# Optimization experiments

Measured on AMD Instinct MI355X. Metric: run time of the kernel, lower is better.

Reference implementation:

```python
import jax, jax.numpy as jnp
import numpy as np

B, S, D = 2, 2048, 2048
H, KVH, DH = 32, 8, 64
G = H // KVH  # num_key_value_groups
SCALE = DH ** -0.5
NEG = -1e9


def rotate_half(x):
    x1, x2 = jnp.split(x, 2, axis=-1)
    return jnp.concatenate([-x2, x1], axis=-1)


def setup_inputs() -> dict:
    key = jax.random.key(0)
    ks = jax.random.split(key, 6)
    hidden_states = jax.random.normal(ks[0], (B, S, D), dtype=jnp.float32)
    # RoPE tables (base 10000), shape [B, S, DH]
    inv_freq = 1.0 / (10000.0 ** (np.arange(0, DH, 2, dtype=np.float32) / DH))
    t = np.arange(S, dtype=np.float32)
    freqs = np.outer(t, inv_freq)                     # [S, DH/2]
    emb = np.concatenate([freqs, freqs], axis=-1)     # [S, DH]
    cos = jnp.broadcast_to(jnp.cos(emb)[None], (B, S, DH)).astype(jnp.float32)
    sin = jnp.broadcast_to(jnp.sin(emb)[None], (B, S, DH)).astype(jnp.float32)
    # additive causal mask [B, 1, S, S]
    causal = np.tril(np.ones((S, S), dtype=bool))
    mask = jnp.asarray(np.where(causal, 0.0, NEG).astype(np.float32))
    attention_mask = jnp.broadcast_to(mask[None, None], (B, 1, S, S))
    std = 0.02
    Wq = jax.random.normal(ks[1], (H * DH, D), dtype=jnp.float32) * std
    Wk = jax.random.normal(ks[2], (KVH * DH, D), dtype=jnp.float32) * std
    Wv = jax.random.normal(ks[3], (KVH * DH, D), dtype=jnp.float32) * std
    Wo = jax.random.normal(ks[4], (D, H * DH), dtype=jnp.float32) * std
    return {"hidden_states": hidden_states, "cos": cos, "sin": sin,
            "attention_mask": attention_mask, "Wq": Wq, "Wk": Wk, "Wv": Wv, "Wo": Wo}


def reference(hidden_states, cos, sin, attention_mask, Wq, Wk, Wv, Wo):
    b, s, d = hidden_states.shape
    # projections -> [B, heads, S, DH]
    q = (hidden_states @ Wq.T).reshape(b, s, H, DH).transpose(0, 2, 1, 3)
    k = (hidden_states @ Wk.T).reshape(b, s, KVH, DH).transpose(0, 2, 1, 3)
    v = (hidden_states @ Wv.T).reshape(b, s, KVH, DH).transpose(0, 2, 1, 3)
    # RoPE (unsqueeze_dim=1)
    c = cos[:, None]  # [B,1,S,DH]
    sn = sin[:, None]
    q = q * c + rotate_half(q) * sn
    k = k * c + rotate_half(k) * sn
    # GQA: repeat kv heads
    k = jnp.repeat(k, G, axis=1)
    v = jnp.repeat(v, G, axis=1)
    scores = jnp.einsum("bhqd,bhkd->bhqk", q, k) * SCALE + attention_mask
    attn = jax.nn.softmax(scores.astype(jnp.float32), axis=-1).astype(q.dtype)
    out = jnp.einsum("bhqk,bhkd->bhqd", attn, v)          # [B,H,S,DH]
    out = out.transpose(0, 2, 1, 3).reshape(b, s, H * DH)  # [B,S,H*DH]
    return out @ Wo.T
```

## Files before the change

kernel.cpp:

```cpp
#include <hip/hip_runtime.h>

typedef unsigned short u16;
typedef __attribute__((ext_vector_type(8))) short s16x8;
typedef __attribute__((ext_vector_type(4))) float f32x4;
typedef __attribute__((ext_vector_type(4))) unsigned short u16x4;

#define MFMA16(a, b, c) __builtin_amdgcn_mfma_f32_16x16x32_bf16(a, b, c, 0, 0, 0)

__device__ __forceinline__ u16 f2bf(float f) {
  unsigned u = __builtin_bit_cast(unsigned, f);
  u += 0x7fffu + ((u >> 16) & 1u);
  return (u16)(u >> 16);
}

__device__ __forceinline__ u16 f2bf_fast(float f) {
  return (u16)((__builtin_bit_cast(unsigned, f) + 0x8000u) >> 16);
}

__device__ __forceinline__ void async16(const void* g, void* l) {
  __builtin_amdgcn_global_load_lds(
      (const __attribute__((address_space(1))) void*)g,
      (__attribute__((address_space(3))) void*)l, 16, 0, 0);
}

__device__ __forceinline__ s16x8 ld8(const u16* p) { return *(const s16x8*)p; }

#define PRE 0.18033688011112042f

__global__ __launch_bounds__(256) void cvt_all(
    const float* __restrict__ X, const float* __restrict__ Wq,
    const float* __restrict__ Wk, const float* __restrict__ Wv,
    const float* __restrict__ Wo, u16* __restrict__ out) {
  long e = (long)(blockIdx.x * 256 + threadIdx.x) * 4;
  const float* src;
  if (e < 8388608L) src = X + e;
  else if (e < 12582912L) src = Wq + (e - 8388608L);
  else if (e < 13631488L) src = Wk + (e - 12582912L);
  else if (e < 14680064L) src = Wv + (e - 13631488L);
  else src = Wo + (e - 14680064L);
  float4 v = *(const float4*)src;
  u16x4 o = {f2bf(v.x), f2bf(v.y), f2bf(v.z), f2bf(v.w)};
  *(u16x4*)(out + e) = o;
}

enum { EPI_QKV = 0, EPI_OUT = 1 };

template <int EPI>
__global__ __launch_bounds__(256) void gemm_nt(
    const u16* __restrict__ A, const u16* __restrict__ Bm,
    const float* __restrict__ cosp, const float* __restrict__ sinp,
    u16* __restrict__ Qo, u16* __restrict__ Ko, u16* __restrict__ Vo,
    float* __restrict__ Co, int K) {
  __shared__ u16 SM[16384];
  const int t = threadIdx.x;
  const int lane = t & 63;
  const int w = t >> 6, wm = w >> 1, wn = w & 1;
  const int quad = lane >> 4, c16 = lane & 15;
  const int m0 = blockIdx.y * 128, n0 = blockIdx.x * 128;

  f32x4 acc[4][4];
  const f32x4 zero = {0.f, 0.f, 0.f, 0.f};
#pragma unroll
  for (int i = 0; i < 4; ++i)
#pragma unroll
    for (int j = 0; j < 4; ++j) acc[i][j] = zero;

  const u16* gA[2];
  const u16* gB[2];
  int lof[2];
#pragma unroll
  for (int p = 0; p < 2; ++p) {
    int c = t + p * 256;
    int dr = c >> 3, k8 = (c & 7) ^ (dr & 7);
    int row = 2 * dr + (k8 >> 2), col = (k8 & 3) * 8;
    gA[p] = A + (size_t)(m0 + row) * K + col;
    gB[p] = Bm + (size_t)(n0 + row) * K + col;
    lof[p] = c * 8;
  }

  int aoff[4], boff[4];
#pragma unroll
  for (int i = 0; i < 4; ++i) {
    int rowA = wm * 64 + i * 16 + c16;
    int drA = rowA >> 1;
    int chA = (((rowA & 1) << 2) | quad) ^ (drA & 7);
    aoff[i] = drA * 64 + chA * 8;
    int rowB = wn * 64 + i * 16 + c16;
    int drB = rowB >> 1;
    int chB = (((rowB & 1) << 2) | quad) ^ (drB & 7);
    boff[i] = 4096 + drB * 64 + chB * 8;
  }

#pragma unroll
  for (int p = 0; p < 2; ++p) {
    async16(gA[p], &SM[lof[p]]);
    async16(gB[p], &SM[4096 + lof[p]]);
  }

  const int niter = K >> 5;
  for (int kt = 0; kt < niter; ++kt) {
    const int cb = (kt & 1) * 8192;
    __syncthreads();
    if (kt + 1 < niter) {
      const int nb = 8192 - cb;
#pragma unroll
      for (int p = 0; p < 2; ++p) {
        gA[p] += 32;
        gB[p] += 32;
        async16(gA[p], &SM[nb + lof[p]]);
        async16(gB[p], &SM[nb + 4096 + lof[p]]);
      }
    }
    s16x8 af[4], bfr[4];
#pragma unroll
    for (int i = 0; i < 4; ++i) af[i] = ld8(&SM[cb + aoff[i]]);
#pragma unroll
    for (int j = 0; j < 4; ++j) bfr[j] = ld8(&SM[cb + boff[j]]);
#pragma unroll
    for (int i = 0; i < 4; ++i)
#pragma unroll
      for (int j = 0; j < 4; ++j) acc[i][j] = MFMA16(af[i], bfr[j], acc[i][j]);
  }

  if (EPI == EPI_OUT) {
#pragma unroll
    for (int i = 0; i < 4; ++i)
#pragma unroll
      for (int r = 0; r < 4; ++r) {
        int m = m0 + wm * 64 + i * 16 + quad * 4 + r;
        float* dst = Co + (size_t)m * 2048 + n0 + wn * 64 + c16;
#pragma unroll
        for (int j = 0; j < 4; ++j) dst[j * 16] = acc[i][j][r];
      }
  } else if (n0 >= 2560) {
    __syncthreads();
#pragma unroll
    for (int i = 0; i < 4; ++i)
#pragma unroll
      for (int r = 0; r < 4; ++r) {
        int sl = wm * 64 + i * 16 + quad * 4 + r;
#pragma unroll
        for (int j = 0; j < 4; ++j) {
          int dl = wn * 64 + j * 16 + c16;
          SM[dl * 128 + (((sl >> 3) ^ (dl & 15)) * 8) + (sl & 7)] =
              f2bf(acc[i][j][r]);
        }
      }
    __syncthreads();
    int bb = m0 >> 11, m0s = m0 & 2047;
#pragma unroll
    for (int p = 0; p < 8; ++p) {
      int q = p * 256 + t;
      int dl = q >> 4, k = q & 15;
      s16x8 vrow = ld8(&SM[dl * 128 + ((k ^ (dl & 15)) * 8)]);
      int nab = n0 + dl;
      int kvh = (nab - 2560) >> 6, dh = nab & 63;
      *(s16x8*)(Vo + ((size_t)(bb * 8 + kvh) * 64 + dh) * 2048 + m0s + k * 8) =
          vrow;
    }
  } else {
    const int nbase = n0 + wn * 64;
#pragma unroll
    for (int i = 0; i < 4; ++i)
#pragma unroll
      for (int r = 0; r < 4; ++r) {
        int m = m0 + wm * 64 + i * 16 + quad * 4 + r;
        int b = m >> 11, s = m & 2047;
        if (nbase < 2048) {
          int h = nbase >> 6;
          size_t base = ((size_t)(b * 32 + h) * 2048 + s) * 64;
#pragma unroll
          for (int j = 0; j < 2; ++j) {
            int d = j * 16 + c16;
            float v1 = acc[i][j][r], v2 = acc[i][j + 2][r];
            float c1 = cosp[m * 64 + d], s1 = sinp[m * 64 + d];
            float c2 = cosp[m * 64 + d + 32], s2 = sinp[m * 64 + d + 32];
            Qo[base + d] = f2bf((v1 * c1 - v2 * s1) * PRE);
            Qo[base + d + 32] = f2bf((v2 * c2 + v1 * s2) * PRE);
          }
        } else {
          int h = (nbase - 2048) >> 6;
          size_t base = ((size_t)(b * 8 + h) * 2048 + s) * 64;
#pragma unroll
          for (int j = 0; j < 2; ++j) {
            int d = j * 16 + c16;
            float v1 = acc[i][j][r], v2 = acc[i][j + 2][r];
            float c1 = cosp[m * 64 + d], s1 = sinp[m * 64 + d];
            float c2 = cosp[m * 64 + d + 32], s2 = sinp[m * 64 + d + 32];
            Ko[base + d] = f2bf(v1 * c1 - v2 * s1);
            Ko[base + d + 32] = f2bf(v2 * c2 + v1 * s2);
          }
        }
      }
  }
}

__global__ __launch_bounds__(256) void attn(const u16* __restrict__ Q,
                                            const u16* __restrict__ Kg,
                                            const u16* __restrict__ Vg,
                                            u16* __restrict__ O) {
  __shared__ u16 Ks[2][4096];
  __shared__ u16 Vs[2][4096];
  __shared__ u16 Ps[8192];
  const int t = threadIdx.x;
  const int lane = t & 63;
  const int w = t >> 6;
  const int quad = lane >> 4, c16 = lane & 15;
  const int bh = blockIdx.y;
  const int b = bh >> 5, h = bh & 31;
  const int kvh = h >> 2;

  const u16* Qbase = Q + ((size_t)(b * 32 + h) * 2048) * 64;
  const u16* Kbase = Kg + ((size_t)(b * 8 + kvh) * 2048) * 64;
  const u16* Vbase = Vg + ((size_t)(b * 8 + kvh) * 64) * 2048;

  const int sr0 = t >> 3, sc0 = ((t & 7) ^ (sr0 & 7)) * 8;
  const int sr1 = (t + 256) >> 3, sc1 = (((t + 256) & 7) ^ (sr1 & 7)) * 8;

  for (int ph = 0; ph < 2; ++ph) {
    const int qt = ph ? 15 - blockIdx.x : blockIdx.x;
    const int q0 = qt * 128;

    s16x8 qa[2][2];
#pragma unroll
    for (int im = 0; im < 2; ++im)
#pragma unroll
      for (int c = 0; c < 2; ++c)
        qa[im][c] = ld8(Qbase + (size_t)(q0 + w * 32 + im * 16 + c16) * 64 +
                        c * 32 + quad * 8);

    f32x4 oacc[2][4];
    const f32x4 zero = {0.f, 0.f, 0.f, 0.f};
    float lacc[2][4];
#pragma unroll
    for (int im = 0; im < 2; ++im)
#pragma unroll
      for (int r = 0; r < 4; ++r) lacc[im][r] = 0.f;
#pragma unroll
    for (int im = 0; im < 2; ++im)
#pragma unroll
      for (int dt = 0; dt < 4; ++dt) oacc[im][dt] = zero;

    const int nkt = 2 * qt + 2;

    __syncthreads();
    {
      const u16* kg = Kbase;
      async16(kg + sr0 * 64 + sc0, &Ks[0][t * 8]);
      async16(kg + sr1 * 64 + sc1, &Ks[0][t * 8 + 2048]);
      async16(Vbase + (size_t)sr0 * 2048 + sc0, &Vs[0][t * 8]);
      async16(Vbase + (size_t)sr1 * 2048 + sc1, &Vs[0][t * 8 + 2048]);
    }

    for (int kt = 0; kt < nkt; ++kt) {
      const int cur = kt & 1;
      __syncthreads();
      if (kt + 1 < nkt) {
        const int nxt = 1 - cur;
        const u16* kg = Kbase + (kt + 1) * 4096;
        async16(kg + sr0 * 64 + sc0, &Ks[nxt][t * 8]);
        async16(kg + sr1 * 64 + sc1, &Ks[nxt][t * 8 + 2048]);
        async16(Vbase + (size_t)sr0 * 2048 + (kt + 1) * 64 + sc0,
                &Vs[nxt][t * 8]);
        async16(Vbase + (size_t)sr1 * 2048 + (kt + 1) * 64 + sc1,
                &Vs[nxt][t * 8 + 2048]);
      }
      const u16* Kb = Ks[cur];
      const u16* Vb = Vs[cur];

#pragma unroll
      for (int im = 0; im < 2; ++im) {
        f32x4 sc[4];
#pragma unroll
        for (int in = 0; in < 4; ++in) sc[in] = zero;
#pragma unroll
        for (int c = 0; c < 2; ++c)
#pragma unroll
          for (int in = 0; in < 4; ++in) {
            s16x8 kf = ld8(&Kb[(in * 16 + c16) * 64 +
                               (((c * 4 + quad) ^ (c16 & 7)) * 8)]);
            sc[in] = MFMA16(qa[im][c], kf, sc[in]);
          }
        const int rbase = q0 + w * 32 + im * 16;
        if (kt * 64 + 63 > rbase) {
#pragma unroll
          for (int in = 0; in < 4; ++in) {
            int kcol = kt * 64 + in * 16 + c16;
#pragma unroll
            for (int r = 0; r < 4; ++r)
              if (kcol > rbase + quad * 4 + r) sc[in][r] = -1e30f;
          }
        }
#pragma unroll
        for (int in = 0; in < 4; ++in)
#pragma unroll
          for (int r = 0; r < 4; ++r) {
            float p = exp2f(sc[in][r]);
            lacc[im][r] += p;
            int row = im * 16 + quad * 4 + r;
            Ps[w * 2048 + row * 64 +
               (((in * 2 + (c16 >> 3)) ^ (row & 7)) * 8) + (c16 & 7)] =
                f2bf_fast(p);
          }
      }

#pragma unroll
      for (int c = 0; c < 2; ++c) {
        const int swz = ((c * 4 + quad) ^ (c16 & 7)) * 8;
        s16x8 pf[2];
#pragma unroll
        for (int im = 0; im < 2; ++im)
          pf[im] = ld8(&Ps[w * 2048 + (im * 16 + c16) * 64 + swz]);
#pragma unroll
        for (int dt = 0; dt < 4; ++dt) {
          s16x8 vf = ld8(&Vb[(dt * 16 + c16) * 64 + swz]);
#pragma unroll
          for (int im = 0; im < 2; ++im)
            oacc[im][dt] = MFMA16(pf[im], vf, oacc[im][dt]);
        }
      }
    }

#pragma unroll
    for (int im = 0; im < 2; ++im) {
      float inv[4];
#pragma unroll
      for (int r = 0; r < 4; ++r) {
        float v = lacc[im][r];
        v += __shfl_xor(v, 1);
        v += __shfl_xor(v, 2);
        v += __shfl_xor(v, 4);
        v += __shfl_xor(v, 8);
        inv[r] = 1.f / v;
      }
#pragma unroll
      for (int dt = 0; dt < 4; ++dt)
#pragma unroll
        for (int r = 0; r < 4; ++r) {
          int s = q0 + w * 32 + im * 16 + quad * 4 + r;
          O[((size_t)(b * 2048 + s)) * 2048 + h * 64 + dt * 16 + c16] =
              f2bf(oacc[im][dt][r] * inv[r]);
        }
    }
  }
}

extern "C" void kernel_launch(void* const* d_in, const int* in_sizes, int n_in,
                              void* d_out, int out_size, void* d_ws,
                              size_t ws_size, hipStream_t stream) {
  const float* X = (const float*)d_in[0];
  const float* cosp = (const float*)d_in[1];
  const float* sinp = (const float*)d_in[2];
  const float* Wq = (const float*)d_in[4];
  const float* Wk = (const float*)d_in[5];
  const float* Wv = (const float*)d_in[6];
  const float* Wo = (const float*)d_in[7];
  float* out = (float*)d_out;

  u16* Xb = (u16*)d_ws;
  u16* Wqkv = Xb + 8388608;
  u16* Wob = Wqkv + 6291456;
  u16* Qr = Wob + 4194304;
  u16* Kr = Qr + 8388608;
  u16* Vt = Kr + 2097152;
  u16* Ob = Vt + 2097152;

  cvt_all<<<18432, 256, 0, stream>>>(X, Wq, Wk, Wv, Wo, Xb);

  gemm_nt<EPI_QKV><<<dim3(24, 32), 256, 0, stream>>>(
      Xb, Wqkv, cosp, sinp, Qr, Kr, Vt, nullptr, 2048);

  attn<<<dim3(8, 64), 256, 0, stream>>>(Qr, Kr, Vt, Ob);

  gemm_nt<EPI_OUT><<<dim3(16, 32), 256, 0, stream>>>(
      Ob, Wob, nullptr, nullptr, nullptr, nullptr, nullptr, out, 2048);
}
```

Baseline: 328.7 us.

## Rewrite attention with 32x32 MFMA transposed scores and shrink output GEMM tile

The attention kernel now uses 32x32x16 bf16 MFMAs and computes transposed scores (K times Q), so each lane owns one query row. That lets the P tile be written to LDS as packed 8-byte bf16 pairs and makes the row-sum reduction a single shuffle. Warps now skip key tiles that lie wholly above the causal diagonal for their 32 rows, and output rows are stored as vector writes. The output-projection GEMM is templated on BN and launched with 64-wide N tiles for more blocks (better occupancy on the 512-tile grid), at the cost of less reuse per block; P is rounded by truncation via perm.

```diff
diff --git a/kernel.cpp b/kernel.cpp
--- a/kernel.cpp
+++ b/kernel.cpp
@@ -3,9 +3,12 @@
 typedef unsigned short u16;
 typedef __attribute__((ext_vector_type(8))) short s16x8;
 typedef __attribute__((ext_vector_type(4))) float f32x4;
+typedef __attribute__((ext_vector_type(16))) float f32x16;
 typedef __attribute__((ext_vector_type(4))) unsigned short u16x4;
+typedef __attribute__((ext_vector_type(2))) unsigned int u32x2;
 
 #define MFMA16(a, b, c) __builtin_amdgcn_mfma_f32_16x16x32_bf16(a, b, c, 0, 0, 0)
+#define MFMA32(a, b, c) __builtin_amdgcn_mfma_f32_32x32x16_bf16(a, b, c, 0, 0, 0)
 
 __device__ __forceinline__ u16 f2bf(float f) {
   unsigned u = __builtin_bit_cast(unsigned, f);
@@ -13,8 +16,9 @@
   return (u16)(u >> 16);
 }
 
-__device__ __forceinline__ u16 f2bf_fast(float f) {
-  return (u16)((__builtin_bit_cast(unsigned, f) + 0x8000u) >> 16);
+__device__ __forceinline__ unsigned pkbf(float lo, float hi) {
+  return __builtin_amdgcn_perm(__builtin_bit_cast(unsigned, hi),
+                               __builtin_bit_cast(unsigned, lo), 0x07060302u);
 }
 
 __device__ __forceinline__ void async16(const void* g, void* l) {
@@ -45,81 +49,94 @@
 
 enum { EPI_QKV = 0, EPI_OUT = 1 };
 
-template <int EPI>
+template <int EPI, int BN>
 __global__ __launch_bounds__(256) void gemm_nt(
     const u16* __restrict__ A, const u16* __restrict__ Bm,
     const float* __restrict__ cosp, const float* __restrict__ sinp,
     u16* __restrict__ Qo, u16* __restrict__ Ko, u16* __restrict__ Vo,
     float* __restrict__ Co, int K) {
-  __shared__ u16 SM[16384];
+  constexpr int BUF = 4096 + BN * 32;
+  constexpr int NJ = BN / 32;
+  constexpr int NB = BN / 64;
+  __shared__ u16 SM[EPI == EPI_QKV ? 16384 : 2 * (4096 + BN * 32)];
   const int t = threadIdx.x;
   const int lane = t & 63;
   const int w = t >> 6, wm = w >> 1, wn = w & 1;
   const int quad = lane >> 4, c16 = lane & 15;
-  const int m0 = blockIdx.y * 128, n0 = blockIdx.x * 128;
-
-  f32x4 acc[4][4];
+  const int m0 = blockIdx.y * 128, n0 = blockIdx.x * BN;
+
+  f32x4 acc[4][NJ];
   const f32x4 zero = {0.f, 0.f, 0.f, 0.f};
 #pragma unroll
   for (int i = 0; i < 4; ++i)
 #pragma unroll
-    for (int j = 0; j < 4; ++j) acc[i][j] = zero;
+    for (int j = 0; j < NJ; ++j) acc[i][j] = zero;
 
   const u16* gA[2];
-  const u16* gB[2];
-  int lof[2];
+  const u16* gB[NB];
+  int lofA[2], lofB[NB];
 #pragma unroll
   for (int p = 0; p < 2; ++p) {
     int c = t + p * 256;
     int dr = c >> 3, k8 = (c & 7) ^ (dr & 7);
-    int row = 2 * dr + (k8 >> 2), col = (k8 & 3) * 8;
-    gA[p] = A + (size_t)(m0 + row) * K + col;
-    gB[p] = Bm + (size_t)(n0 + row) * K + col;
-    lof[p] = c * 8;
-  }
-
-  int aoff[4], boff[4];
+    gA[p] = A + (size_t)(m0 + 2 * dr + (k8 >> 2)) * K + (k8 & 3) * 8;
+    lofA[p] = c * 8;
+  }
+#pragma unroll
+  for (int p = 0; p < NB; ++p) {
+    int c = t + p * 256;
+    int dr = c >> 3, k8 = (c & 7) ^ (dr & 7);
+    gB[p] = Bm + (size_t)(n0 + 2 * dr + (k8 >> 2)) * K + (k8 & 3) * 8;
+    lofB[p] = 4096 + c * 8;
+  }
+
+  int aoff[4], boff[NJ];
 #pragma unroll
   for (int i = 0; i < 4; ++i) {
     int rowA = wm * 64 + i * 16 + c16;
     int drA = rowA >> 1;
     int chA = (((rowA & 1) << 2) | quad) ^ (drA & 7);
     aoff[i] = drA * 64 + chA * 8;
-    int rowB = wn * 64 + i * 16 + c16;
+  }
+#pragma unroll
+  for (int j = 0; j < NJ; ++j) {
+    int rowB = wn * (BN / 2) + j * 16 + c16;
     int drB = rowB >> 1;
     int chB = (((rowB & 1) << 2) | quad) ^ (drB & 7);
-    boff[i] = 4096 + drB * 64 + chB * 8;
-  }
-
-#pragma unroll
-  for (int p = 0; p < 2; ++p) {
-    async16(gA[p], &SM[lof[p]]);
-    async16(gB[p], &SM[4096 + lof[p]]);
-  }
+    boff[j] = 4096 + drB * 64 + chB * 8;
+  }
+
+#pragma unroll
+  for (int p = 0; p < 2; ++p) async16(gA[p], &SM[lofA[p]]);
+#pragma unroll
+  for (int p = 0; p < NB; ++p) async16(gB[p], &SM[lofB[p]]);
 
   const int niter = K >> 5;
   for (int kt = 0; kt < niter; ++kt) {
-    const int cb = (kt & 1) * 8192;
+    const int cb = (kt & 1) * BUF;
     __syncthreads();
     if (kt + 1 < niter) {
-      const int nb = 8192 - cb;
+      const int nb = BUF - cb;
 #pragma unroll
       for (int p = 0; p < 2; ++p) {
         gA[p] += 32;
+        async16(gA[p], &SM[nb + lofA[p]]);
+      }
+#pragma unroll
+      for (int p = 0; p < NB; ++p) {
         gB[p] += 32;
-        async16(gA[p], &SM[nb + lof[p]]);
-        async16(gB[p], &SM[nb + 4096 + lof[p]]);
-      }
-    }
-    s16x8 af[4], bfr[4];
+        async16(gB[p], &SM[nb + lofB[p]]);
+      }
+    }
+    s16x8 af[4], bfr[NJ];
 #pragma unroll
     for (int i = 0; i < 4; ++i) af[i] = ld8(&SM[cb + aoff[i]]);
 #pragma unroll
-    for (int j = 0; j < 4; ++j) bfr[j] = ld8(&SM[cb + boff[j]]);
+    for (int j = 0; j < NJ; ++j) bfr[j] = ld8(&SM[cb + boff[j]]);
 #pragma unroll
     for (int i = 0; i < 4; ++i)
 #pragma unroll
-      for (int j = 0; j < 4; ++j) acc[i][j] = MFMA16(af[i], bfr[j], acc[i][j]);
+      for (int j = 0; j < NJ; ++j) acc[i][j] = MFMA16(af[i], bfr[j], acc[i][j]);
   }
 
   if (EPI == EPI_OUT) {
@@ -128,9 +145,9 @@
 #pragma unroll
       for (int r = 0; r < 4; ++r) {
         int m = m0 + wm * 64 + i * 16 + quad * 4 + r;
-        float* dst = Co + (size_t)m * 2048 + n0 + wn * 64 + c16;
-#pragma unroll
-        for (int j = 0; j < 4; ++j) dst[j * 16] = acc[i][j][r];
+        float* dst = Co + (size_t)m * 2048 + n0 + wn * (BN / 2) + c16;
+#pragma unroll
+        for (int j = 0; j < NJ; ++j) dst[j * 16] = acc[i][j][r];
       }
   } else if (n0 >= 2560) {
     __syncthreads();
@@ -205,7 +222,8 @@
   const int t = threadIdx.x;
   const int lane = t & 63;
   const int w = t >> 6;
-  const int quad = lane >> 4, c16 = lane & 15;
+  const int l31 = lane & 31;
+  const int lh = lane >> 5;
   const int bh = blockIdx.y;
   const int b = bh >> 5, h = bh & 31;
   const int kvh = h >> 2;
@@ -217,37 +235,38 @@
   const int sr0 = t >> 3, sc0 = ((t & 7) ^ (sr0 & 7)) * 8;
   const int sr1 = (t + 256) >> 3, sc1 = (((t + 256) & 7) ^ (sr1 & 7)) * 8;
 
+  int swz[4];
+#pragma unroll
+  for (int dep = 0; dep < 4; ++dep)
+    swz[dep] = l31 * 64 + (((dep * 2 + lh) ^ (l31 & 7)) * 8);
+  int wof[8];
+#pragma unroll
+  for (int c8 = 0; c8 < 8; ++c8)
+    wof[c8] = w * 2048 + l31 * 64 + ((c8 ^ (l31 & 7)) * 8) + 4 * lh;
+
   for (int ph = 0; ph < 2; ++ph) {
     const int qt = ph ? 15 - blockIdx.x : blockIdx.x;
     const int q0 = qt * 128;
-
-    s16x8 qa[2][2];
-#pragma unroll
-    for (int im = 0; im < 2; ++im)
-#pragma unroll
-      for (int c = 0; c < 2; ++c)
-        qa[im][c] = ld8(Qbase + (size_t)(q0 + w * 32 + im * 16 + c16) * 64 +
-                        c * 32 + quad * 8);
-
-    f32x4 oacc[2][4];
-    const f32x4 zero = {0.f, 0.f, 0.f, 0.f};
-    float lacc[2][4];
-#pragma unroll
-    for (int im = 0; im < 2; ++im)
-#pragma unroll
-      for (int r = 0; r < 4; ++r) lacc[im][r] = 0.f;
-#pragma unroll
-    for (int im = 0; im < 2; ++im)
-#pragma unroll
-      for (int dt = 0; dt < 4; ++dt) oacc[im][dt] = zero;
+    const int qw = q0 + w * 32;
+
+    s16x8 qb[4];
+#pragma unroll
+    for (int dep = 0; dep < 4; ++dep)
+      qb[dep] = ld8(Qbase + (size_t)(qw + l31) * 64 + dep * 16 + lh * 8);
+
+    f32x16 osum[2];
+    float lacc = 0.f;
+#pragma unroll
+    for (int mt = 0; mt < 2; ++mt)
+#pragma unroll
+      for (int r = 0; r < 16; ++r) osum[mt][r] = 0.f;
 
     const int nkt = 2 * qt + 2;
 
     __syncthreads();
     {
-      const u16* kg = Kbase;
-      async16(kg + sr0 * 64 + sc0, &Ks[0][t * 8]);
-      async16(kg + sr1 * 64 + sc1, &Ks[0][t * 8 + 2048]);
+      async16(Kbase + sr0 * 64 + sc0, &Ks[0][t * 8]);
+      async16(Kbase + sr1 * 64 + sc1, &Ks[0][t * 8 + 2048]);
       async16(Vbase + (size_t)sr0 * 2048 + sc0, &Vs[0][t * 8]);
       async16(Vbase + (size_t)sr1 * 2048 + sc1, &Vs[0][t * 8 + 2048]);
     }
@@ -265,81 +284,80 @@
         async16(Vbase + (size_t)sr1 * 2048 + (kt + 1) * 64 + sc1,
                 &Vs[nxt][t * 8 + 2048]);
       }
+      if (kt * 64 > qw + 31) continue;
       const u16* Kb = Ks[cur];
       const u16* Vb = Vs[cur];
 
-#pragma unroll
-      for (int im = 0; im < 2; ++im) {
-        f32x4 sc[4];
-#pragma unroll
-        for (int in = 0; in < 4; ++in) sc[in] = zero;
-#pragma unroll
-        for (int c = 0; c < 2; ++c)
-#pragma unroll
-          for (int in = 0; in < 4; ++in) {
-            s16x8 kf = ld8(&Kb[(in * 16 + c16) * 64 +
-                               (((c * 4 + quad) ^ (c16 & 7)) * 8)]);
-            sc[in] = MFMA16(qa[im][c], kf, sc[in]);
+      f32x16 sT[2];
+#pragma unroll
+      for (int mt = 0; mt < 2; ++mt) {
+        const int tilebase = kt * 64 + mt * 32;
+        if (tilebase > qw + 31) continue;
+#pragma unroll
+        for (int r = 0; r < 16; ++r) sT[mt][r] = 0.f;
+#pragma unroll
+        for (int dep = 0; dep < 4; ++dep) {
+          s16x8 kf = ld8(&Kb[mt * 2048 + swz[dep]]);
+          sT[mt] = MFMA32(kf, qb[dep], sT[mt]);
+        }
+      }
+#pragma unroll
+      for (int mt = 0; mt < 2; ++mt) {
+        const int tilebase = kt * 64 + mt * 32;
+        const bool live = tilebase <= qw + 31;
+        if (live && tilebase + 31 > qw) {
+          const int qa = qw + l31;
+#pragma unroll
+          for (int r = 0; r < 16; ++r) {
+            int key = tilebase + (r & 3) + 8 * (r >> 2) + 4 * lh;
+            if (key > qa) sT[mt][r] = -1e30f;
           }
-        const int rbase = q0 + w * 32 + im * 16;
-        if (kt * 64 + 63 > rbase) {
-#pragma unroll
-          for (int in = 0; in < 4; ++in) {
-            int kcol = kt * 64 + in * 16 + c16;
-#pragma unroll
-            for (int r = 0; r < 4; ++r)
-              if (kcol > rbase + quad * 4 + r) sc[in][r] = -1e30f;
+        }
+#pragma unroll
+        for (int rq = 0; rq < 4; ++rq) {
+          u32x2 pv;
+          if (live) {
+            float p0 = exp2f(sT[mt][rq * 4 + 0]);
+            float p1 = exp2f(sT[mt][rq * 4 + 1]);
+            float p2 = exp2f(sT[mt][rq * 4 + 2]);
+            float p3 = exp2f(sT[mt][rq * 4 + 3]);
+            lacc += (p0 + p1) + (p2 + p3);
+            pv[0] = pkbf(p0, p1);
+            pv[1] = pkbf(p2, p3);
+          } else {
+            pv[0] = 0u;
+            pv[1] = 0u;
           }
-        }
-#pragma unroll
-        for (int in = 0; in < 4; ++in)
-#pragma unroll
-          for (int r = 0; r < 4; ++r) {
-            float p = exp2f(sc[in][r]);
-            lacc[im][r] += p;
-            int row = im * 16 + quad * 4 + r;
-            Ps[w * 2048 + row * 64 +
-               (((in * 2 + (c16 >> 3)) ^ (row & 7)) * 8) + (c16 & 7)] =
-                f2bf_fast(p);
-          }
-      }
-
-#pragma unroll
-      for (int c = 0; c < 2; ++c) {
-        const int swz = ((c * 4 + quad) ^ (c16 & 7)) * 8;
-        s16x8 pf[2];
-#pragma unroll
-        for (int im = 0; im < 2; ++im)
-          pf[im] = ld8(&Ps[w * 2048 + (im * 16 + c16) * 64 + swz]);
-#pragma unroll
-        for (int dt = 0; dt < 4; ++dt) {
-          s16x8 vf = ld8(&Vb[(dt * 16 + c16) * 64 + swz]);
-#pragma unroll
-          for (int im = 0; im < 2; ++im)
-            oacc[im][dt] = MFMA16(pf[im], vf, oacc[im][dt]);
-        }
-      }
-    }
-
-#pragma unroll
-    for (int im = 0; im < 2; ++im) {
-      float inv[4];
-#pragma unroll
-      for (int r = 0; r < 4; ++r) {
-        float v = lacc[im][r];
-        v += __shfl_xor(v, 1);
-        v += __shfl_xor(v, 2);
-        v += __shfl_xor(v, 4);
-        v += __shfl_xor(v, 8);
-        inv[r] = 1.f / v;
-      }
-#pragma unroll
-      for (int dt = 0; dt < 4; ++dt)
-#pragma unroll
-        for (int r = 0; r < 4; ++r) {
-          int s = q0 + w * 32 + im * 16 + quad * 4 + r;
-          O[((size_t)(b * 2048 + s)) * 2048 + h * 64 + dt * 16 + c16] =
-              f2bf(oacc[im][dt][r] * inv[r]);
+          *(u32x2*)(&Ps[wof[mt * 4 + rq]]) = pv;
+        }
+      }
+      s16x8 pf[4];
+#pragma unroll
+      for (int dep = 0; dep < 4; ++dep)
+        pf[dep] = ld8(&Ps[w * 2048 + swz[dep]]);
+#pragma unroll
+      for (int mt2 = 0; mt2 < 2; ++mt2)
+#pragma unroll
+        for (int dep = 0; dep < 4; ++dep) {
+          s16x8 vf = ld8(&Vb[mt2 * 2048 + swz[dep]]);
+          osum[mt2] = MFMA32(vf, pf[dep], osum[mt2]);
+        }
+    }
+
+    {
+      float lt = lacc + __shfl_xor(lacc, 32);
+      float inv = 1.f / lt;
+      u16* obase = O + ((size_t)(b * 2048 + qw + l31)) * 2048 + h * 64;
+#pragma unroll
+      for (int mt2 = 0; mt2 < 2; ++mt2)
+#pragma unroll
+        for (int rq = 0; rq < 4; ++rq) {
+          float v0 = osum[mt2][rq * 4 + 0] * inv;
+          float v1 = osum[mt2][rq * 4 + 1] * inv;
+          float v2 = osum[mt2][rq * 4 + 2] * inv;
+          float v3 = osum[mt2][rq * 4 + 3] * inv;
+          u16x4 ov = {f2bf(v0), f2bf(v1), f2bf(v2), f2bf(v3)};
+          *(u16x4*)(obase + mt2 * 32 + rq * 8 + 4 * lh) = ov;
         }
     }
   }
@@ -367,11 +385,11 @@
 
   cvt_all<<<18432, 256, 0, stream>>>(X, Wq, Wk, Wv, Wo, Xb);
 
-  gemm_nt<EPI_QKV><<<dim3(24, 32), 256, 0, stream>>>(
+  gemm_nt<EPI_QKV, 128><<<dim3(24, 32), 256, 0, stream>>>(
       Xb, Wqkv, cosp, sinp, Qr, Kr, Vt, nullptr, 2048);
 
   attn<<<dim3(8, 64), 256, 0, stream>>>(Qr, Kr, Vt, Ob);
 
-  gemm_nt<EPI_OUT><<<dim3(16, 32), 256, 0, stream>>>(
+  gemm_nt<EPI_OUT, 64><<<dim3(32, 32), 256, 0, stream>>>(
       Ob, Wob, nullptr, nullptr, nullptr, nullptr, nullptr, out, 2048);
 }
```

Result: slower. 346.7 us (+5.5%).
